# Performance work log

Hardware: AMD Instinct MI355X
Metric: run time of the kernel (lower is better)

## Reference

```python
import jax, jax.numpy as jnp
import numpy as np

K_DIM = 1024
HEADS = 16


def setup_inputs() -> dict:
    key = jax.random.key(0)
    ks = jax.random.split(key, 6)
    b, t, k = 2, 2048, K_DIM
    scale = 1.0 / np.sqrt(k)
    x = jax.random.normal(ks[0], (b, t, k), dtype=jnp.float32)
    # nn.Linear stores weight as [out, in]; y = x @ W.T
    Wq = jax.random.normal(ks[1], (k, k), dtype=jnp.float32) * scale
    Wk = jax.random.normal(ks[2], (k, k), dtype=jnp.float32) * scale
    Wv = jax.random.normal(ks[3], (k, k), dtype=jnp.float32) * scale
    Wo = jax.random.normal(ks[4], (k, k), dtype=jnp.float32) * scale
    bo = jax.random.normal(ks[5], (k,), dtype=jnp.float32) * scale
    return {"x": x, "Wq": Wq, "Wk": Wk, "Wv": Wv, "Wo": Wo, "bo": bo}


def reference(x, Wq, Wk, Wv, Wo, bo):
    b, t, k = x.shape
    h = HEADS
    hd = k // h
    q = (x @ Wq.T).reshape(b, t, h, hd)
    kk = (x @ Wk.T).reshape(b, t, h, hd)
    v = (x @ Wv.T).reshape(b, t, h, hd)
    # scores: [b, h, t, t]
    scores = jnp.einsum('bqhd,bkhd->bhqk', q, kk) / jnp.sqrt(jnp.float32(hd))
    w = jax.nn.softmax(scores, axis=-1)
    out = jnp.einsum('bhqk,bkhd->bqhd', w, v).reshape(b, t, k)
    return out @ Wo.T + bo
```

## Files before the change

### kernel.cpp

```cpp
#include <hip/hip_runtime.h>
#include <stdint.h>
#include <stddef.h>

#define TB 2048
#define KDIM 1024
#define NH 16
#define HD 64

typedef __attribute__((ext_vector_type(8))) __bf16 bf16x8;
typedef __attribute__((ext_vector_type(2))) float f32x2;
typedef __attribute__((ext_vector_type(4))) float f32x4;
typedef __attribute__((ext_vector_type(16))) float f32x16;
typedef __attribute__((ext_vector_type(4))) unsigned short u16x4;
typedef __attribute__((ext_vector_type(8))) unsigned short u16x8;
typedef __attribute__((ext_vector_type(4))) unsigned u32x4;
typedef __attribute__((ext_vector_type(2))) unsigned u32x2;

static __device__ __forceinline__ unsigned short f2bf(float f) {
  unsigned u = __builtin_bit_cast(unsigned, f);
  return (unsigned short)((u + 0x7FFFu + ((u >> 16) & 1u)) >> 16);
}

static __device__ __forceinline__ bf16x8 ld_frag(const unsigned short* p) {
  u16x8 v = *(const u16x8*)p;
  return __builtin_bit_cast(bf16x8, v);
}

static __device__ __forceinline__ void gload_lds16(const void* g, void* l) {
  auto gp = (const __attribute__((address_space(1))) unsigned int*)(uintptr_t)g;
  auto lp = (__attribute__((address_space(3))) unsigned int*)(unsigned int)(uintptr_t)l;
  __builtin_amdgcn_global_load_lds(gp, lp, 16, 0, 0);
}

static __device__ __forceinline__ float fast_exp2(float x) {
  float r;
  asm("v_exp_f32 %0, %1" : "=v"(r) : "v"(x));
  return r;
}

static __device__ __forceinline__ unsigned cvt_pk(float a, float b) {
  unsigned r;
  asm("v_cvt_pk_bf16_f32 %0, %1, %2" : "=v"(r) : "v"(a), "v"(b));
  return r;
}

static __device__ __forceinline__ u32x2 permswap(unsigned a, unsigned b) {
  return __builtin_amdgcn_permlane32_swap(a, b, false, false);
}

static __device__ __forceinline__ f32x2 pk_fma(f32x2 a, f32x2 b, f32x2 c) {
  f32x2 d;
  asm("v_pk_fma_f32 %0, %1, %2, %3" : "=v"(d) : "v"(a), "v"(b), "v"(c));
  return d;
}
static __device__ __forceinline__ f32x2 pk_add(f32x2 a, f32x2 b) {
  f32x2 d;
  asm("v_pk_add_f32 %0, %1, %2" : "=v"(d) : "v"(a), "v"(b));
  return d;
}
static __device__ __forceinline__ float max3f(float a, float b, float c) {
  float d;
  asm("v_max3_f32 %0, %1, %2, %3" : "=v"(d) : "v"(a), "v"(b), "v"(c));
  return d;
}

__global__ __launch_bounds__(256) void k_cvt_all(
    const float* __restrict__ x, const float* __restrict__ Wq,
    const float* __restrict__ Wk, const float* __restrict__ Wv,
    const float* __restrict__ Wo, unsigned short* __restrict__ xb,
    unsigned short* __restrict__ wb) {
  int bb = blockIdx.x;
  const float* src;
  unsigned short* dst;
  int i;
  if (bb < 2048) {
    src = x; dst = xb; i = bb * 256 + threadIdx.x;
  } else {
    int wsel = (bb - 2048) >> 9;
    src = (wsel == 0) ? Wq : (wsel == 1) ? Wk : (wsel == 2) ? Wv : Wo;
    dst = wb + (size_t)wsel * (KDIM * KDIM);
    i = ((bb - 2048) & 511) * 256 + threadIdx.x;
  }
  const float4* p = (const float4*)src + (size_t)i * 2;
  float4 a = p[0], b = p[1];
  u16x8 o;
  o[0] = f2bf(a.x); o[1] = f2bf(a.y); o[2] = f2bf(a.z); o[3] = f2bf(a.w);
  o[4] = f2bf(b.x); o[5] = f2bf(b.y); o[6] = f2bf(b.z); o[7] = f2bf(b.w);
  *((u16x8*)dst + i) = o;
}

template <int MODE>
static __device__ __forceinline__ void gemm_body(
    const unsigned short* __restrict__ A, const unsigned short* __restrict__ W,
    unsigned short* __restrict__ Cb, float* __restrict__ Cf,
    const float* __restrict__ bias, int by, int bx,
    unsigned short* As, unsigned short* Bs) {
  const int K = KDIM, N = KDIM;
  int tid = threadIdx.x, lane = tid & 63, wid = tid >> 6;
  int r = lane & 15, g = lane >> 4;
  int wm = wid >> 1, wn = wid & 1;

  f32x4 acc[4][4];
#pragma unroll
  for (int m = 0; m < 4; ++m)
#pragma unroll
    for (int n = 0; n < 4; ++n) acc[m][n] = (f32x4){0.f, 0.f, 0.f, 0.f};

  const unsigned short* Ag = A + (size_t)(by * 128) * K;
  const unsigned short* Wg = W + (size_t)(bx * 128) * K;

  for (int k0 = 0; k0 < K; k0 += 64) {
#pragma unroll
    for (int it = 0; it < 4; ++it) {
      int base = it * 256 + wid * 64;
      int c = base + lane;
      int rr = c >> 3;
      int blk = (c & 7) ^ (rr & 7);
      gload_lds16(Ag + (size_t)rr * K + k0 + blk * 8, &As[base * 8]);
      gload_lds16(Wg + (size_t)rr * K + k0 + blk * 8, &Bs[base * 8]);
    }
    __syncthreads();
#pragma unroll
    for (int ks = 0; ks < 2; ++ks) {
      bf16x8 af[4], bf[4];
#pragma unroll
      for (int m = 0; m < 4; ++m) {
        int row = wm * 64 + m * 16 + r;
        af[m] = ld_frag(&As[row * 64 + ((ks * 4 + g) ^ (r & 7)) * 8]);
      }
#pragma unroll
      for (int n = 0; n < 4; ++n) {
        int row = wn * 64 + n * 16 + r;
        bf[n] = ld_frag(&Bs[row * 64 + ((ks * 4 + g) ^ (r & 7)) * 8]);
      }
      __builtin_amdgcn_s_setprio(1);
#pragma unroll
      for (int m = 0; m < 4; ++m)
#pragma unroll
        for (int n = 0; n < 4; ++n)
          acc[m][n] = __builtin_amdgcn_mfma_f32_16x16x32_bf16(af[m], bf[n], acc[m][n], 0, 0, 0);
      __builtin_amdgcn_s_setprio(0);
    }
    __syncthreads();
  }

#pragma unroll
  for (int m = 0; m < 4; ++m)
#pragma unroll
    for (int n = 0; n < 4; ++n) {
      int col = bx * 128 + wn * 64 + n * 16 + r;
      if (MODE == 2) {
        int hq = col >> 6, dq = col & 63;
        int row0 = by * 128 + wm * 64 + m * 16 + g * 4;
        int bq = row0 >> 11, tq = row0 & 2047;
        u16x4 pv;
#pragma unroll
        for (int j = 0; j < 4; ++j) pv[j] = f2bf(acc[m][n][j]);
        *(u16x4*)&Cb[(((size_t)(bq * NH + hq)) * HD + dq) * TB + tq] = pv;
      } else {
#pragma unroll
        for (int j = 0; j < 4; ++j) {
          int row = by * 128 + wm * 64 + m * 16 + g * 4 + j;
          if (MODE == 0)
            Cb[(size_t)row * N + col] = f2bf(acc[m][n][j]);
          else
            Cf[(size_t)row * N + col] = acc[m][n][j] + bias[col];
        }
      }
    }
}

__global__ __launch_bounds__(256) void k_gemm_qkv(
    const unsigned short* __restrict__ X,
    const unsigned short* __restrict__ Wq, const unsigned short* __restrict__ Wk,
    const unsigned short* __restrict__ Wv,
    unsigned short* __restrict__ Q, unsigned short* __restrict__ Kp,
    unsigned short* __restrict__ Vt) {
  __shared__ __align__(16) unsigned short As[8192];
  __shared__ __align__(16) unsigned short Bs[8192];
  int idx = blockIdx.x;
  int by = idx / 24, bxx = idx % 24;
  int which = bxx >> 3, bx = bxx & 7;
  if (which == 2) {
    gemm_body<2>(X, Wv, Vt, nullptr, nullptr, by, bx, As, Bs);
  } else {
    const unsigned short* W = which ? Wk : Wq;
    unsigned short* C = which ? Kp : Q;
    gemm_body<0>(X, W, C, nullptr, nullptr, by, bx, As, Bs);
  }
}

__global__ __launch_bounds__(256) void k_gemm_out(
    const unsigned short* __restrict__ AO, const unsigned short* __restrict__ Wo,
    float* __restrict__ out, const float* __restrict__ bias) {
  __shared__ __align__(16) unsigned short As[8192];
  __shared__ __align__(16) unsigned short Bs[8192];
  int by = blockIdx.x >> 3, bx = blockIdx.x & 7;
  gemm_body<1>(AO, Wo, nullptr, out, bias, by, bx, As, Bs);
}

__global__ __launch_bounds__(512, 4) void k_attn(
    const unsigned short* __restrict__ Q, const unsigned short* __restrict__ Kp,
    const unsigned short* __restrict__ Vt, unsigned short* __restrict__ AO) {
  __shared__ __align__(16) unsigned short Ks[2][2][4096];
  __shared__ __align__(16) unsigned short Vs[2][2][4096];

  int qt = blockIdx.x & 15, bh = blockIdx.x >> 4;
  int b = bh >> 4, h = bh & 15;
  int tid = threadIdx.x, lane = tid & 63, w = tid >> 6;
  int wl = w & 3, half = w >> 2;
  int q = lane & 31, hh = lane >> 5;
  const float LOG2E = 1.44269504f;
  const int HT = (TB / 64) / 2;

  const unsigned short* Qp =
      Q + ((size_t)(b * TB + qt * 128 + wl * 32 + q)) * KDIM + h * HD;
  bf16x8 qf[4];
#pragma unroll
  for (int f = 0; f < 4; ++f) qf[f] = ld_frag(&Qp[16 * f + 8 * hh]);

  f32x16 o0, o1;
#pragma unroll
  for (int i = 0; i < 16; ++i) { o0[i] = 0.f; o1[i] = 0.f; }
  float m_run = -1e30f, l_run = 0.f;

  const unsigned short* Kbase = Kp + (size_t)(b * TB) * KDIM + h * HD;
  const unsigned short* Vbase = Vt + (size_t)bh * HD * TB;

  auto stage = [&](int kt, int buf) {
#pragma unroll
    for (int it = 0; it < 2; ++it) {
      int base = it * 256 + wl * 64;
      int c = base + lane;
      int rr = c >> 3;
      int blk = (c & 7) ^ (rr & 7);
      gload_lds16(Kbase + (size_t)(kt * 64 + rr) * KDIM + blk * 8,
                  &Ks[half][buf][base * 8]);
      gload_lds16(Vbase + (size_t)rr * TB + kt * 64 + blk * 8,
                  &Vs[half][buf][base * 8]);
    }
  };

  stage(half * HT, 0);
  __syncthreads();
  int cur = 0;

  for (int t = 0; t < HT; ++t) {
    if (t + 1 < HT) stage(half * HT + t + 1, cur ^ 1);

    const unsigned short* Kc = &Ks[half][cur][0];
    f32x16 st[2];
    __builtin_amdgcn_s_setprio(1);
#pragma unroll
    for (int g = 0; g < 2; ++g) {
#pragma unroll
      for (int i = 0; i < 16; ++i) st[g][i] = 0.f;
#pragma unroll
      for (int f = 0; f < 4; ++f) {
        int row = g * 32 + q;
        int bl = (2 * f + hh) ^ (row & 7);
        bf16x8 kf = ld_frag(&Kc[row * 64 + bl * 8]);
        st[g] = __builtin_amdgcn_mfma_f32_32x32x16_bf16(kf, qf[f], st[g], 0, 0, 0);
      }
    }
    __builtin_amdgcn_s_setprio(0);

    float m0 = max3f(st[0][0], st[0][1], st[0][2]);
    float m1 = max3f(st[0][3], st[0][4], st[0][5]);
    float m2 = max3f(st[0][6], st[0][7], st[0][8]);
    float m3 = max3f(st[0][9], st[0][10], st[0][11]);
    float m4 = max3f(st[0][12], st[0][13], st[0][14]);
    float m5 = max3f(st[0][15], st[1][0], st[1][1]);
    float m6 = max3f(st[1][2], st[1][3], st[1][4]);
    float m7 = max3f(st[1][5], st[1][6], st[1][7]);
    float m8 = max3f(st[1][8], st[1][9], st[1][10]);
    float m9 = max3f(st[1][11], st[1][12], st[1][13]);
    float u0 = max3f(m0, m1, m2);
    float u1 = max3f(m3, m4, m5);
    float u2 = max3f(m6, m7, m8);
    float u3 = max3f(m9, st[1][14], st[1][15]);
    float pm = fmaxf(fmaxf(u0, u1), fmaxf(u2, u3));
    pm = fmaxf(pm, __shfl_xor(pm, 32));
    float spm = pm * 0.125f;
    if (!__all(spm <= m_run + 8.f)) {
      float mnew = fmaxf(m_run, spm);
      float sc = fast_exp2((m_run - mnew) * LOG2E);
      m_run = mnew;
      l_run *= sc;
#pragma unroll
      for (int p = 0; p < 16; ++p) {
        float scp = __shfl(sc, (p & 3) + 8 * (p >> 2) + 4 * hh);
        o0[p] *= scp;
        o1[p] *= scp;
      }
    }

    float c1 = 0.125f * LOG2E, c2 = m_run * LOG2E;
    f32x2 c1v; c1v[0] = c1; c1v[1] = c1;
    f32x2 c2v; c2v[0] = -c2; c2v[1] = -c2;
    f32x2 rsv; rsv[0] = 0.f; rsv[1] = 0.f;
    bf16x8 pa[4];
#pragma unroll
    for (int g = 0; g < 2; ++g) {
      unsigned d[8];
#pragma unroll
      for (int i = 0; i < 8; ++i) {
        f32x2 p; p[0] = st[g][2 * i]; p[1] = st[g][2 * i + 1];
        p = pk_fma(p, c1v, c2v);
        f32x2 e; e[0] = fast_exp2(p[0]); e[1] = fast_exp2(p[1]);
        rsv = pk_add(rsv, e);
        d[i] = cvt_pk(e[0], e[1]);
      }
      u32x2 r1 = permswap(d[0], d[2]);
      u32x2 r2 = permswap(d[1], d[3]);
      u32x2 r3 = permswap(d[4], d[6]);
      u32x2 r4 = permswap(d[5], d[7]);
      u32x4 t0; t0[0] = r1.x; t0[1] = r2.x; t0[2] = r1.y; t0[3] = r2.y;
      u32x4 t1; t1[0] = r3.x; t1[1] = r4.x; t1[2] = r3.y; t1[3] = r4.y;
      pa[2 * g]     = __builtin_bit_cast(bf16x8, t0);
      pa[2 * g + 1] = __builtin_bit_cast(bf16x8, t1);
    }
    float rs = rsv[0] + rsv[1];
    rs += __shfl_xor(rs, 32);
    l_run += rs;

    const unsigned short* Vc = &Vs[half][cur][0];
    __builtin_amdgcn_s_setprio(1);
#pragma unroll
    for (int s = 0; s < 4; ++s) {
      int bl = (2 * s + hh) ^ (q & 7);
      bf16x8 v0 = ld_frag(&Vc[q * 64 + bl * 8]);
      bf16x8 v1 = ld_frag(&Vc[(32 + q) * 64 + bl * 8]);
      o0 = __builtin_amdgcn_mfma_f32_32x32x16_bf16(pa[s], v0, o0, 0, 0, 0);
      o1 = __builtin_amdgcn_mfma_f32_32x32x16_bf16(pa[s], v1, o1, 0, 0, 0);
    }
    __builtin_amdgcn_s_setprio(0);

    __syncthreads();
    cur ^= 1;
  }

  float* Osw = (float*)&Vs[0][0][0];
  float* MLb = (float*)&Ks[0][0][0];
  if (half) {
#pragma unroll
    for (int p = 0; p < 16; ++p) {
      Osw[p * 256 + wl * 64 + lane]        = o0[p];
      Osw[(16 + p) * 256 + wl * 64 + lane] = o1[p];
    }
    if (!hh) {
      MLb[wl * 32 + q]       = m_run;
      MLb[128 + wl * 32 + q] = l_run;
    }
  }
  __syncthreads();
  if (!half) {
    float m2r = MLb[wl * 32 + q], l2 = MLb[128 + wl * 32 + q];
    float mm = fmaxf(m_run, m2r);
    float ea = fast_exp2((m_run - mm) * LOG2E);
    float eb = fast_exp2((m2r - mm) * LOG2E);
    float il = 1.f / (l_run * ea + l2 * eb);
#pragma unroll
    for (int p = 0; p < 16; ++p) {
      int qr = (p & 3) + 8 * (p >> 2) + 4 * hh;
      float a  = __shfl(ea, qr);
      float bb = __shfl(eb, qr);
      float ip = __shfl(il, qr);
      float v0 = (o0[p] * a + Osw[p * 256 + wl * 64 + lane] * bb) * ip;
      float v1 = (o1[p] * a + Osw[(16 + p) * 256 + wl * 64 + lane] * bb) * ip;
      int row = qt * 128 + wl * 32 + qr;
      size_t base = ((size_t)(b * TB + row)) * KDIM + h * HD;
      AO[base + q]      = f2bf(v0);
      AO[base + 32 + q] = f2bf(v1);
    }
  }
}

extern "C" void kernel_launch(void* const* d_in, const int* in_sizes, int n_in,
                              void* d_out, int out_size, void* d_ws, size_t ws_size,
                              hipStream_t stream) {
  const float* x  = (const float*)d_in[0];
  const float* Wq = (const float*)d_in[1];
  const float* Wk = (const float*)d_in[2];
  const float* Wv = (const float*)d_in[3];
  const float* Wo = (const float*)d_in[4];
  const float* bo = (const float*)d_in[5];

  char* ws = (char*)d_ws;
  const size_t MB = 1 << 20;
  unsigned short* xb  = (unsigned short*)(ws + 0 * MB);
  unsigned short* wqb = (unsigned short*)(ws + 8 * MB);
  unsigned short* wkb = (unsigned short*)(ws + 10 * MB);
  unsigned short* wvb = (unsigned short*)(ws + 12 * MB);
  unsigned short* wob = (unsigned short*)(ws + 14 * MB);
  unsigned short* Qb  = (unsigned short*)(ws + 16 * MB);
  unsigned short* Kb  = (unsigned short*)(ws + 24 * MB);
  unsigned short* Vtb = (unsigned short*)(ws + 32 * MB);
  unsigned short* AOb = (unsigned short*)(ws + 40 * MB);

  k_cvt_all<<<4096, 256, 0, stream>>>(x, Wq, Wk, Wv, Wo, xb, wqb);
  k_gemm_qkv<<<32 * 24, 256, 0, stream>>>(xb, wqb, wkb, wvb, Qb, Kb, Vtb);
  k_attn<<<512, 512, 0, stream>>>(Qb, Kb, Vtb, AOb);
  k_gemm_out<<<256, 256, 0, stream>>>(AOb, wob, (float*)d_out, bo);
}
```

Measured before the change: 120.2 us.

## Split each KV tile across wave halves with triple-buffered shared staging

Both wave groups now walk every 64-key tile together. Each group computes scores for one 32-key half of the tile, where before each group took half of the whole sequence with its own buffers. K/V staging moves to a shared triple buffer with a two-tile-ahead prefetch, explicit vmcnt waits and a raw s_barrier in place of __syncthreads. This halves the staging issue per thread and lets loads run further ahead of compute. Block index ordering also changes so consecutive blocks cover different batch-head pairs. The risks are twice as many barriers per key, and a final merge of two partial softmax states that each saw interleaved key subsets.

New measurement: 121.8 us. No clear change (+1.3%).

```diff
diff --git a/kernel.cpp b/kernel.cpp
--- a/kernel.cpp
+++ b/kernel.cpp
@@ -202,16 +202,17 @@
 __global__ __launch_bounds__(512, 4) void k_attn(
     const unsigned short* __restrict__ Q, const unsigned short* __restrict__ Kp,
     const unsigned short* __restrict__ Vt, unsigned short* __restrict__ AO) {
-  __shared__ __align__(16) unsigned short Ks[2][2][4096];
-  __shared__ __align__(16) unsigned short Vs[2][2][4096];
-
-  int qt = blockIdx.x & 15, bh = blockIdx.x >> 4;
+  __shared__ __align__(16) unsigned short LDSb[6 * 4096];
+  unsigned short* KsB = LDSb;
+  unsigned short* VsB = LDSb + 3 * 4096;
+
+  int qt = blockIdx.x >> 5, bh = blockIdx.x & 31;
   int b = bh >> 4, h = bh & 15;
   int tid = threadIdx.x, lane = tid & 63, w = tid >> 6;
-  int wl = w & 3, half = w >> 2;
+  int wl = w & 3, kh = w >> 2;
   int q = lane & 31, hh = lane >> 5;
   const float LOG2E = 1.44269504f;
-  const int HT = (TB / 64) / 2;
+  const int NT = TB / 64;
 
   const unsigned short* Qp =
       Q + ((size_t)(b * TB + qt * 128 + wl * 32 + q)) * KDIM + h * HD;
@@ -224,62 +225,51 @@
   for (int i = 0; i < 16; ++i) { o0[i] = 0.f; o1[i] = 0.f; }
   float m_run = -1e30f, l_run = 0.f;
 
-  const unsigned short* Kbase = Kp + (size_t)(b * TB) * KDIM + h * HD;
-  const unsigned short* Vbase = Vt + (size_t)bh * HD * TB;
+  int c = w * 64 + lane;
+  int rr = c >> 3;
+  int blk = (c & 7) ^ (rr & 7);
+  const unsigned short* Kg =
+      Kp + (size_t)(b * TB) * KDIM + h * HD + (size_t)rr * KDIM + blk * 8;
+  const unsigned short* Vg =
+      Vt + (size_t)bh * HD * TB + (size_t)rr * TB + blk * 8;
+  int ldst = w * 512;
 
   auto stage = [&](int kt, int buf) {
-#pragma unroll
-    for (int it = 0; it < 2; ++it) {
-      int base = it * 256 + wl * 64;
-      int c = base + lane;
-      int rr = c >> 3;
-      int blk = (c & 7) ^ (rr & 7);
-      gload_lds16(Kbase + (size_t)(kt * 64 + rr) * KDIM + blk * 8,
-                  &Ks[half][buf][base * 8]);
-      gload_lds16(Vbase + (size_t)rr * TB + kt * 64 + blk * 8,
-                  &Vs[half][buf][base * 8]);
-    }
+    gload_lds16(Kg + (size_t)kt * 64 * KDIM, &KsB[buf * 4096 + ldst]);
+    gload_lds16(Vg + kt * 64, &VsB[buf * 4096 + ldst]);
   };
 
-  stage(half * HT, 0);
-  __syncthreads();
-  int cur = 0;
-
-  for (int t = 0; t < HT; ++t) {
-    if (t + 1 < HT) stage(half * HT + t + 1, cur ^ 1);
-
-    const unsigned short* Kc = &Ks[half][cur][0];
-    f32x16 st[2];
+  stage(0, 0);
+  stage(1, 1);
+  asm volatile("s_waitcnt vmcnt(2)" ::: "memory");
+  __builtin_amdgcn_s_barrier();
+  __builtin_amdgcn_sched_barrier(0);
+
+  for (int t = 0; t < NT; ++t) {
+    int cur = t % 3;
+    bool pf = (t + 2 < NT);
+    if (pf) stage(t + 2, (t + 2) % 3);
+
+    const unsigned short* Kc = &KsB[cur * 4096];
+    f32x16 st;
+#pragma unroll
+    for (int i = 0; i < 16; ++i) st[i] = 0.f;
     __builtin_amdgcn_s_setprio(1);
 #pragma unroll
-    for (int g = 0; g < 2; ++g) {
-#pragma unroll
-      for (int i = 0; i < 16; ++i) st[g][i] = 0.f;
-#pragma unroll
-      for (int f = 0; f < 4; ++f) {
-        int row = g * 32 + q;
-        int bl = (2 * f + hh) ^ (row & 7);
-        bf16x8 kf = ld_frag(&Kc[row * 64 + bl * 8]);
-        st[g] = __builtin_amdgcn_mfma_f32_32x32x16_bf16(kf, qf[f], st[g], 0, 0, 0);
-      }
+    for (int f = 0; f < 4; ++f) {
+      int row = kh * 32 + q;
+      int bl = (2 * f + hh) ^ (q & 7);
+      bf16x8 kf = ld_frag(&Kc[row * 64 + bl * 8]);
+      st = __builtin_amdgcn_mfma_f32_32x32x16_bf16(kf, qf[f], st, 0, 0, 0);
     }
     __builtin_amdgcn_s_setprio(0);
 
-    float m0 = max3f(st[0][0], st[0][1], st[0][2]);
-    float m1 = max3f(st[0][3], st[0][4], st[0][5]);
-    float m2 = max3f(st[0][6], st[0][7], st[0][8]);
-    float m3 = max3f(st[0][9], st[0][10], st[0][11]);
-    float m4 = max3f(st[0][12], st[0][13], st[0][14]);
-    float m5 = max3f(st[0][15], st[1][0], st[1][1]);
-    float m6 = max3f(st[1][2], st[1][3], st[1][4]);
-    float m7 = max3f(st[1][5], st[1][6], st[1][7]);
-    float m8 = max3f(st[1][8], st[1][9], st[1][10]);
-    float m9 = max3f(st[1][11], st[1][12], st[1][13]);
-    float u0 = max3f(m0, m1, m2);
-    float u1 = max3f(m3, m4, m5);
-    float u2 = max3f(m6, m7, m8);
-    float u3 = max3f(m9, st[1][14], st[1][15]);
-    float pm = fmaxf(fmaxf(u0, u1), fmaxf(u2, u3));
+    float m0 = max3f(st[0], st[1], st[2]);
+    float m1 = max3f(st[3], st[4], st[5]);
+    float m2 = max3f(st[6], st[7], st[8]);
+    float m3 = max3f(st[9], st[10], st[11]);
+    float m4 = max3f(st[12], st[13], st[14]);
+    float pm = fmaxf(max3f(m0, m1, m2), max3f(m3, m4, st[15]));
     pm = fmaxf(pm, __shfl_xor(pm, 32));
     float spm = pm * 0.125f;
     if (!__all(spm <= m_run + 8.f)) {
@@ -299,50 +289,52 @@
     f32x2 c1v; c1v[0] = c1; c1v[1] = c1;
     f32x2 c2v; c2v[0] = -c2; c2v[1] = -c2;
     f32x2 rsv; rsv[0] = 0.f; rsv[1] = 0.f;
-    bf16x8 pa[4];
-#pragma unroll
-    for (int g = 0; g < 2; ++g) {
-      unsigned d[8];
-#pragma unroll
-      for (int i = 0; i < 8; ++i) {
-        f32x2 p; p[0] = st[g][2 * i]; p[1] = st[g][2 * i + 1];
-        p = pk_fma(p, c1v, c2v);
-        f32x2 e; e[0] = fast_exp2(p[0]); e[1] = fast_exp2(p[1]);
-        rsv = pk_add(rsv, e);
-        d[i] = cvt_pk(e[0], e[1]);
-      }
-      u32x2 r1 = permswap(d[0], d[2]);
-      u32x2 r2 = permswap(d[1], d[3]);
-      u32x2 r3 = permswap(d[4], d[6]);
-      u32x2 r4 = permswap(d[5], d[7]);
-      u32x4 t0; t0[0] = r1.x; t0[1] = r2.x; t0[2] = r1.y; t0[3] = r2.y;
-      u32x4 t1; t1[0] = r3.x; t1[1] = r4.x; t1[2] = r3.y; t1[3] = r4.y;
-      pa[2 * g]     = __builtin_bit_cast(bf16x8, t0);
-      pa[2 * g + 1] = __builtin_bit_cast(bf16x8, t1);
-    }
+    unsigned d[8];
+#pragma unroll
+    for (int i = 0; i < 8; ++i) {
+      f32x2 p; p[0] = st[2 * i]; p[1] = st[2 * i + 1];
+      p = pk_fma(p, c1v, c2v);
+      f32x2 e; e[0] = fast_exp2(p[0]); e[1] = fast_exp2(p[1]);
+      rsv = pk_add(rsv, e);
+      d[i] = cvt_pk(e[0], e[1]);
+    }
+    u32x2 r1 = permswap(d[0], d[2]);
+    u32x2 r2 = permswap(d[1], d[3]);
+    u32x2 r3 = permswap(d[4], d[6]);
+    u32x2 r4 = permswap(d[5], d[7]);
+    u32x4 t0; t0[0] = r1.x; t0[1] = r2.x; t0[2] = r1.y; t0[3] = r2.y;
+    u32x4 t1; t1[0] = r3.x; t1[1] = r4.x; t1[2] = r3.y; t1[3] = r4.y;
+    bf16x8 pa0 = __builtin_bit_cast(bf16x8, t0);
+    bf16x8 pa1 = __builtin_bit_cast(bf16x8, t1);
     float rs = rsv[0] + rsv[1];
     rs += __shfl_xor(rs, 32);
     l_run += rs;
 
-    const unsigned short* Vc = &Vs[half][cur][0];
+    const unsigned short* Vc = &VsB[cur * 4096];
     __builtin_amdgcn_s_setprio(1);
-#pragma unroll
-    for (int s = 0; s < 4; ++s) {
-      int bl = (2 * s + hh) ^ (q & 7);
-      bf16x8 v0 = ld_frag(&Vc[q * 64 + bl * 8]);
-      bf16x8 v1 = ld_frag(&Vc[(32 + q) * 64 + bl * 8]);
-      o0 = __builtin_amdgcn_mfma_f32_32x32x16_bf16(pa[s], v0, o0, 0, 0, 0);
-      o1 = __builtin_amdgcn_mfma_f32_32x32x16_bf16(pa[s], v1, o1, 0, 0, 0);
+    {
+      int bl0 = (kh * 4 + hh) ^ (q & 7);
+      int bl1 = (kh * 4 + 2 + hh) ^ (q & 7);
+      bf16x8 v00 = ld_frag(&Vc[q * 64 + bl0 * 8]);
+      bf16x8 v01 = ld_frag(&Vc[(32 + q) * 64 + bl0 * 8]);
+      bf16x8 v10 = ld_frag(&Vc[q * 64 + bl1 * 8]);
+      bf16x8 v11 = ld_frag(&Vc[(32 + q) * 64 + bl1 * 8]);
+      o0 = __builtin_amdgcn_mfma_f32_32x32x16_bf16(pa0, v00, o0, 0, 0, 0);
+      o1 = __builtin_amdgcn_mfma_f32_32x32x16_bf16(pa0, v01, o1, 0, 0, 0);
+      o0 = __builtin_amdgcn_mfma_f32_32x32x16_bf16(pa1, v10, o0, 0, 0, 0);
+      o1 = __builtin_amdgcn_mfma_f32_32x32x16_bf16(pa1, v11, o1, 0, 0, 0);
     }
     __builtin_amdgcn_s_setprio(0);
 
-    __syncthreads();
-    cur ^= 1;
-  }
-
-  float* Osw = (float*)&Vs[0][0][0];
-  float* MLb = (float*)&Ks[0][0][0];
-  if (half) {
+    if (pf) asm volatile("s_waitcnt vmcnt(2)" ::: "memory");
+    else    asm volatile("s_waitcnt vmcnt(0)" ::: "memory");
+    __builtin_amdgcn_s_barrier();
+    __builtin_amdgcn_sched_barrier(0);
+  }
+
+  float* Osw = (float*)LDSb;
+  float* MLb = ((float*)LDSb) + 8192;
+  if (kh) {
 #pragma unroll
     for (int p = 0; p < 16; ++p) {
       Osw[p * 256 + wl * 64 + lane]        = o0[p];
@@ -354,7 +346,7 @@
     }
   }
   __syncthreads();
-  if (!half) {
+  if (!kh) {
     float m2r = MLb[wl * 32 + q], l2 = MLb[128 + wl * 32 + q];
     float mm = fmaxf(m_run, m2r);
     float ea = fast_exp2((m_run - mm) * LOG2E);
```
